# Performance work log

Measured on AMD Instinct MI355X. Metric: run time of the kernel, lower is better.

## Reference

```python
import jax, jax.numpy as jnp
from jax import lax
import numpy as np

# larq-style ste_sign: forward sign (with sign(0)=+1), straight-through grad clipped to |x|<=1
@jax.custom_vjp
def ste_sign(x):
    return jnp.where(x >= 0, 1.0, -1.0).astype(x.dtype)

def _ste_fwd(x):
    return ste_sign(x), x

def _ste_bwd(x, g):
    return (g * (jnp.abs(x) <= 1.0).astype(g.dtype),)

ste_sign.defvjp(_ste_fwd, _ste_bwd)


def setup_inputs() -> dict:
    key = jax.random.key(0)
    k1, k2 = jax.random.split(key)
    B, H, Wd, Cin = 16, 256, 256, 32
    M, kh, kw, Cout = 4, 3, 3, 32
    x = jax.random.normal(k1, (B, H, Wd, Cin), dtype=jnp.float32)
    W = jax.random.normal(k2, (M, kh, kw, Cin, Cout), dtype=jnp.float32)
    b = jnp.zeros((M, Cout), dtype=jnp.float32)
    return {"x": x, "W": W, "b": b}


def reference(x, W, b):
    # Multibin: sum_{m} QuantConv2D_m(x).  Each branch binarizes the SAME input,
    # so sum of convs == one conv with the sum of the binarized kernels (fused).
    xq = ste_sign(x)                 # [B,H,W,Cin], values in {-1,+1}
    wq = ste_sign(W)                 # [M,kh,kw,Cin,Cout]
    w_sum = wq.sum(axis=0)           # [kh,kw,Cin,Cout]
    y = lax.conv_general_dilated(
        xq, w_sum,
        window_strides=(1, 1),
        padding="SAME",
        dimension_numbers=("NHWC", "HWIO", "NHWC"),
    )
    return y + b.sum(axis=0)         # [B,H,W,Cout]
```

## Files before the change

kernel.cpp:

```cpp
#include <hip/hip_runtime.h>


#define RH     16
#define NSTAGE 130
#define PITCH  40
#define SLOT   (NSTAGE * PITCH)

typedef __attribute__((ext_vector_type(8)))  short  short8;
typedef __attribute__((ext_vector_type(8)))  __bf16 bf16x8;
typedef __attribute__((ext_vector_type(16))) float  f32x16;

__device__ __forceinline__ unsigned int pack2(float a, float b, bool ok) {
    unsigned int lo = ok ? ((a >= 0.0f) ? 0x3F80u : 0xBF80u) : 0u;
    unsigned int hi = ok ? ((b >= 0.0f) ? 0x3F80u : 0xBF80u) : 0u;
    return lo | (hi << 16);
}

__global__ void prep_kernel(const float* __restrict__ W, const float* __restrict__ bias,
                            unsigned short* __restrict__ wsT, float* __restrict__ bsum) {
    int t = blockIdx.x * 256 + threadIdx.x;
    if (t < 9216) {
        int k   = t >> 5;
        int co  = t & 31;
        int tap = k >> 5;
        int ci  = k & 31;
        float s = 0.0f;
        #pragma unroll
        for (int m = 0; m < 4; ++m) {
            float w = W[(m * 9 + tap) * 1024 + ci * 32 + co];
            s += (w >= 0.0f) ? 1.0f : -1.0f;
        }
        unsigned int u = __builtin_bit_cast(unsigned int, s);
        wsT[co * 288 + k] = (unsigned short)(u >> 16);
    }
    if (t < 32) {
        float s = 0.0f;
        #pragma unroll
        for (int m = 0; m < 4; ++m) s += bias[m * 32 + t];
        bsum[t] = s;
    }
}

__device__ __forceinline__ void stage_row(const float* __restrict__ x,
                                          unsigned short* __restrict__ dst,
                                          int bimg, int c0, int absrow, int tid) {
    bool rowok = (absrow >= 0) && (absrow < 256);
    const float* rowp = x + (long)((bimg * 256 + absrow) * 256) * 32;
    #pragma unroll
    for (int p = 0; p < 5; ++p) {
        int f = tid + p * 256;
        int pix = f >> 3, ch = f & 7;
        if (pix < NSTAGE) {
            int col = c0 - 1 + pix;
            bool ok = rowok && (col >= 0) && (col < 256);
            float4 v = ok ? *(const float4*)(rowp + col * 32 + ch * 4)
                          : make_float4(0.f, 0.f, 0.f, 0.f);
            *(uint2*)(dst + pix * PITCH + ch * 4) =
                make_uint2(pack2(v.x, v.y, ok), pack2(v.z, v.w, ok));
        }
    }
}

__global__ __launch_bounds__(256) void conv_kernel(const float* __restrict__ x,
                                                   const unsigned short* __restrict__ wsT,
                                                   const float* __restrict__ bsum,
                                                   float* __restrict__ out) {
    __shared__ unsigned short lds[4 * SLOT];

    const int tid  = threadIdx.x;
    const int lane = tid & 63;
    const int wv   = tid >> 6;
    const int lrow = lane & 31;
    const int lk   = lane >> 5;

    const int bs   = blockIdx.x;
    const int c0   = (bs & 1) * 128;
    const int r0   = ((bs >> 1) & 15) * RH;
    const int bimg = bs >> 5;

    bf16x8 bfrag[18];
    #pragma unroll
    for (int t = 0; t < 18; ++t)
        bfrag[t] = *(const bf16x8*)(wsT + lrow * 288 + t * 16 + lk * 8);
    const float bsv = bsum[lrow];

    #pragma unroll
    for (int pre = 0; pre < 3; ++pre)
        stage_row(x, lds + pre * SLOT, bimg, c0, r0 - 1 + pre, tid);
    __syncthreads();

    const int a_base = (wv * 32 + lrow) * PITCH + lk * 8;

    for (int i = 0; i < RH; ++i) {
        const int r = r0 + i;
        const bool do_pf = (i < RH - 1);
        const int absrow = r + 2;
        const bool rowok = do_pf && (absrow < 256);
        const float* rowp = x + (long)((bimg * 256 + absrow) * 256) * 32;

        float4 buf[5];
        #pragma unroll
        for (int p = 0; p < 5; ++p) {
            int f = tid + p * 256;
            int pix = f >> 3, ch = f & 7;
            int col = c0 - 1 + pix;
            bool ok = rowok && (pix < NSTAGE) && (col >= 0) && (col < 256);
            buf[p] = ok ? *(const float4*)(rowp + col * 32 + ch * 4)
                        : make_float4(0.f, 0.f, 0.f, 0.f);
        }

        f32x16 acc = {};
        #pragma unroll
        for (int dh = 0; dh < 3; ++dh) {
            const unsigned short* sb = lds + ((i + dh) & 3) * SLOT + a_base;
            #pragma unroll
            for (int dw = 0; dw < 3; ++dw) {
                #pragma unroll
                for (int hf = 0; hf < 2; ++hf) {
                    bf16x8 a = *(const bf16x8*)(sb + dw * PITCH + hf * 16);
                    acc = __builtin_amdgcn_mfma_f32_32x32x16_bf16(
                              a, bfrag[(dh * 3 + dw) * 2 + hf], acc, 0, 0, 0);
                }
            }
        }

        float* op = out + ((long)((bimg * 256 + r) * 256 + c0 + wv * 32)) * 32 + lrow;
        #pragma unroll
        for (int reg = 0; reg < 16; ++reg) {
            int pr = (reg & 3) + 8 * (reg >> 2) + 4 * lk;
            op[pr * 32] = acc[reg] + bsv;
        }

        if (do_pf) {
            unsigned short* dst = lds + ((i + 3) & 3) * SLOT;
            #pragma unroll
            for (int p = 0; p < 5; ++p) {
                int f = tid + p * 256;
                int pix = f >> 3, ch = f & 7;
                if (pix < NSTAGE) {
                    int col = c0 - 1 + pix;
                    bool ok = (absrow < 256) && (col >= 0) && (col < 256);
                    *(uint2*)(dst + pix * PITCH + ch * 4) =
                        make_uint2(pack2(buf[p].x, buf[p].y, ok),
                                   pack2(buf[p].z, buf[p].w, ok));
                }
            }
        }
        __syncthreads();
    }
}

extern "C" void kernel_launch(void* const* d_in, const int* in_sizes, int n_in,
                              void* d_out, int out_size, void* d_ws, size_t ws_size,
                              hipStream_t stream) {
    const float* x    = (const float*)d_in[0];
    const float* W    = (const float*)d_in[1];
    const float* bias = (const float*)d_in[2];
    float* out = (float*)d_out;

    unsigned short* wsT = (unsigned short*)d_ws;
    float* bsum = (float*)((char*)d_ws + 18432);

    prep_kernel<<<36, 256, 0, stream>>>(W, bias, wsT, bsum);
    conv_kernel<<<512, 256, 0, stream>>>(x, wsT, bsum, out);
}
```

Measured before the change: 263.3 us.

## Switch conv to int8 MFMA with single-wave blocks and no barriers

Binarized activations and summed weights are now stored as int8 and multiplied with the i32 32x32x32 int8 MFMA, which halves the LDS footprint and the number of MFMA issues relative to bf16. Each block becomes a single 64-lane wavefront covering 32 columns by 8 rows, so the per-row __syncthreads is removed and far more blocks are launched. Output stores become nontemporal. The cost is more halo redundancy, since 34 staged columns serve 32 outputs, and each block's row pipeline is shorter.

```diff
diff --git a/kernel.cpp b/kernel.cpp
--- a/kernel.cpp
+++ b/kernel.cpp
@@ -1,23 +1,25 @@
 #include <hip/hip_runtime.h>
 
 
-#define RH     16
-#define NSTAGE 130
-#define PITCH  40
-#define SLOT   (NSTAGE * PITCH)
+#define RH      8
+#define NSTAGE  34
+#define PITCHB  48
+#define SLOTB   (NSTAGE * PITCHB)
 
-typedef __attribute__((ext_vector_type(8)))  short  short8;
-typedef __attribute__((ext_vector_type(8)))  __bf16 bf16x8;
-typedef __attribute__((ext_vector_type(16))) float  f32x16;
+typedef __attribute__((ext_vector_type(4)))  int i32x4;
+typedef __attribute__((ext_vector_type(16))) int i32x16;
 
-__device__ __forceinline__ unsigned int pack2(float a, float b, bool ok) {
-    unsigned int lo = ok ? ((a >= 0.0f) ? 0x3F80u : 0xBF80u) : 0u;
-    unsigned int hi = ok ? ((b >= 0.0f) ? 0x3F80u : 0xBF80u) : 0u;
-    return lo | (hi << 16);
+__device__ __forceinline__ unsigned int pack4(float4 v, bool ok) {
+    if (!ok) return 0u;
+    unsigned r = (v.x >= 0.0f) ? 0x01u : 0xFFu;
+    r |= ((v.y >= 0.0f) ? 0x01u : 0xFFu) << 8;
+    r |= ((v.z >= 0.0f) ? 0x01u : 0xFFu) << 16;
+    r |= ((v.w >= 0.0f) ? 0x01u : 0xFFu) << 24;
+    return r;
 }
 
 __global__ void prep_kernel(const float* __restrict__ W, const float* __restrict__ bias,
-                            unsigned short* __restrict__ wsT, float* __restrict__ bsum) {
+                            signed char* __restrict__ wsT, float* __restrict__ bsum) {
     int t = blockIdx.x * 256 + threadIdx.x;
     if (t < 9216) {
         int k   = t >> 5;
@@ -30,8 +32,7 @@
             float w = W[(m * 9 + tap) * 1024 + ci * 32 + co];
             s += (w >= 0.0f) ? 1.0f : -1.0f;
         }
-        unsigned int u = __builtin_bit_cast(unsigned int, s);
-        wsT[co * 288 + k] = (unsigned short)(u >> 16);
+        wsT[co * 288 + k] = (signed char)(int)s;
     }
     if (t < 32) {
         float s = 0.0f;
@@ -41,56 +42,52 @@
     }
 }
 
-__device__ __forceinline__ void stage_row(const float* __restrict__ x,
-                                          unsigned short* __restrict__ dst,
-                                          int bimg, int c0, int absrow, int tid) {
-    bool rowok = (absrow >= 0) && (absrow < 256);
-    const float* rowp = x + (long)((bimg * 256 + absrow) * 256) * 32;
-    #pragma unroll
-    for (int p = 0; p < 5; ++p) {
-        int f = tid + p * 256;
-        int pix = f >> 3, ch = f & 7;
-        if (pix < NSTAGE) {
-            int col = c0 - 1 + pix;
-            bool ok = rowok && (col >= 0) && (col < 256);
-            float4 v = ok ? *(const float4*)(rowp + col * 32 + ch * 4)
-                          : make_float4(0.f, 0.f, 0.f, 0.f);
-            *(uint2*)(dst + pix * PITCH + ch * 4) =
-                make_uint2(pack2(v.x, v.y, ok), pack2(v.z, v.w, ok));
-        }
-    }
-}
+__global__ __launch_bounds__(64, 4) void conv_kernel(const float* __restrict__ x,
+                                                     const signed char* __restrict__ wsT,
+                                                     const float* __restrict__ bsum,
+                                                     float* __restrict__ out) {
+    __shared__ __align__(16) unsigned char lds[4 * SLOTB];
 
-__global__ __launch_bounds__(256) void conv_kernel(const float* __restrict__ x,
-                                                   const unsigned short* __restrict__ wsT,
-                                                   const float* __restrict__ bsum,
-                                                   float* __restrict__ out) {
-    __shared__ unsigned short lds[4 * SLOT];
-
-    const int tid  = threadIdx.x;
-    const int lane = tid & 63;
-    const int wv   = tid >> 6;
+    const int lane = threadIdx.x;
     const int lrow = lane & 31;
     const int lk   = lane >> 5;
 
     const int bs   = blockIdx.x;
-    const int c0   = (bs & 1) * 128;
-    const int r0   = ((bs >> 1) & 15) * RH;
-    const int bimg = bs >> 5;
+    const int c0   = (bs & 7) * 32;
+    const int r0   = ((bs >> 3) & 31) * RH;
+    const int bimg = bs >> 8;
 
-    bf16x8 bfrag[18];
+    i32x4 bfrag[9];
     #pragma unroll
-    for (int t = 0; t < 18; ++t)
-        bfrag[t] = *(const bf16x8*)(wsT + lrow * 288 + t * 16 + lk * 8);
+    for (int t = 0; t < 9; ++t)
+        bfrag[t] = *(const i32x4*)(wsT + lrow * 288 + t * 32 + lk * 16);
     const float bsv = bsum[lrow];
 
     #pragma unroll
-    for (int pre = 0; pre < 3; ++pre)
-        stage_row(x, lds + pre * SLOT, bimg, c0, r0 - 1 + pre, tid);
-    __syncthreads();
+    for (int pre = 0; pre < 3; ++pre) {
+        const int absrow = r0 - 1 + pre;
+        const bool rowok = (absrow >= 0) && (absrow < 256);
+        const float* rowp = x + (long)((bimg * 256 + absrow) * 256) * 32;
+        unsigned char* dst = lds + pre * SLOTB;
+        #pragma unroll
+        for (int p = 0; p < 3; ++p) {
+            int f = lane + p * 64;
+            int pix = f >> 2, ch = f & 3;
+            if (pix < NSTAGE) {
+                int col = c0 - 1 + pix;
+                bool ok = rowok && (col >= 0) && (col < 256);
+                const float4* pp = (const float4*)(rowp + (long)col * 32 + ch * 8);
+                float4 v0 = ok ? pp[0] : make_float4(0.f, 0.f, 0.f, 0.f);
+                float4 v1 = ok ? pp[1] : make_float4(0.f, 0.f, 0.f, 0.f);
+                *(uint2*)(dst + pix * PITCHB + ch * 8) =
+                    make_uint2(pack4(v0, ok), pack4(v1, ok));
+            }
+        }
+    }
 
-    const int a_base = (wv * 32 + lrow) * PITCH + lk * 8;
+    const int a_off = lrow * PITCHB + lk * 16;
 
+    #pragma unroll 4
     for (int i = 0; i < RH; ++i) {
         const int r = r0 + i;
         const bool do_pf = (i < RH - 1);
@@ -98,55 +95,51 @@
         const bool rowok = do_pf && (absrow < 256);
         const float* rowp = x + (long)((bimg * 256 + absrow) * 256) * 32;
 
-        float4 buf[5];
+        float4 v0[3], v1[3];
         #pragma unroll
-        for (int p = 0; p < 5; ++p) {
-            int f = tid + p * 256;
-            int pix = f >> 3, ch = f & 7;
+        for (int p = 0; p < 3; ++p) {
+            int f = lane + p * 64;
+            int pix = f >> 2, ch = f & 3;
             int col = c0 - 1 + pix;
             bool ok = rowok && (pix < NSTAGE) && (col >= 0) && (col < 256);
-            buf[p] = ok ? *(const float4*)(rowp + col * 32 + ch * 4)
-                        : make_float4(0.f, 0.f, 0.f, 0.f);
+            const float4* pp = (const float4*)(rowp + (long)col * 32 + ch * 8);
+            v0[p] = ok ? pp[0] : make_float4(0.f, 0.f, 0.f, 0.f);
+            v1[p] = ok ? pp[1] : make_float4(0.f, 0.f, 0.f, 0.f);
         }
 
-        f32x16 acc = {};
+        i32x16 acc = {};
         #pragma unroll
         for (int dh = 0; dh < 3; ++dh) {
-            const unsigned short* sb = lds + ((i + dh) & 3) * SLOT + a_base;
+            const unsigned char* sb = lds + ((i + dh) & 3) * SLOTB + a_off;
             #pragma unroll
             for (int dw = 0; dw < 3; ++dw) {
-                #pragma unroll
-                for (int hf = 0; hf < 2; ++hf) {
-                    bf16x8 a = *(const bf16x8*)(sb + dw * PITCH + hf * 16);
-                    acc = __builtin_amdgcn_mfma_f32_32x32x16_bf16(
-                              a, bfrag[(dh * 3 + dw) * 2 + hf], acc, 0, 0, 0);
+                i32x4 a = *(const i32x4*)(sb + dw * PITCHB);
+                acc = __builtin_amdgcn_mfma_i32_32x32x32_i8(a, bfrag[dh * 3 + dw],
+                                                            acc, 0, 0, 0);
+            }
+        }
+
+        float* op = out + ((long)((bimg * 256 + r) * 256 + c0)) * 32 + lrow;
+        #pragma unroll
+        for (int reg = 0; reg < 16; ++reg) {
+            int pr = (reg & 3) + 8 * (reg >> 2) + 4 * lk;
+            __builtin_nontemporal_store((float)acc[reg] + bsv, op + pr * 32);
+        }
+
+        if (do_pf) {
+            unsigned char* dst = lds + ((i + 3) & 3) * SLOTB;
+            #pragma unroll
+            for (int p = 0; p < 3; ++p) {
+                int f = lane + p * 64;
+                int pix = f >> 2, ch = f & 3;
+                if (pix < NSTAGE) {
+                    int col = c0 - 1 + pix;
+                    bool ok = (absrow < 256) && (col >= 0) && (col < 256);
+                    *(uint2*)(dst + pix * PITCHB + ch * 8) =
+                        make_uint2(pack4(v0[p], ok), pack4(v1[p], ok));
                 }
             }
         }
-
-        float* op = out + ((long)((bimg * 256 + r) * 256 + c0 + wv * 32)) * 32 + lrow;
-        #pragma unroll
-        for (int reg = 0; reg < 16; ++reg) {
-            int pr = (reg & 3) + 8 * (reg >> 2) + 4 * lk;
-            op[pr * 32] = acc[reg] + bsv;
-        }
-
-        if (do_pf) {
-            unsigned short* dst = lds + ((i + 3) & 3) * SLOT;
-            #pragma unroll
-            for (int p = 0; p < 5; ++p) {
-                int f = tid + p * 256;
-                int pix = f >> 3, ch = f & 7;
-                if (pix < NSTAGE) {
-                    int col = c0 - 1 + pix;
-                    bool ok = (absrow < 256) && (col >= 0) && (col < 256);
-                    *(uint2*)(dst + pix * PITCH + ch * 4) =
-                        make_uint2(pack2(buf[p].x, buf[p].y, ok),
-                                   pack2(buf[p].z, buf[p].w, ok));
-                }
-            }
-        }
-        __syncthreads();
     }
 }
 
@@ -158,9 +151,9 @@
     const float* bias = (const float*)d_in[2];
     float* out = (float*)d_out;
 
-    unsigned short* wsT = (unsigned short*)d_ws;
-    float* bsum = (float*)((char*)d_ws + 18432);
+    signed char* wsT = (signed char*)d_ws;
+    float* bsum = (float*)((char*)d_ws + 9216);
 
     prep_kernel<<<36, 256, 0, stream>>>(W, bias, wsT, bsum);
-    conv_kernel<<<512, 256, 0, stream>>>(x, wsT, bsum, out);
+    conv_kernel<<<4096, 64, 0, stream>>>(x, wsT, bsum, out);
 }
```

After: 248.9 us. 1.06x faster.
